# Kernel tuning notes

Measured on AMD Instinct MI355X. Metric: run time of the kernel, lower is better.

Reference implementation:

```python
import jax, jax.numpy as jnp
import numpy as np


def setup_inputs() -> dict:
    key = jax.random.key(0)
    ks = jax.random.split(key, 8)
    N, S, C, V = 64, 50, 100, 10000
    return {
        "logits": jax.random.normal(ks[0], (N, S, C), dtype=jnp.float32),
        "target": jax.random.randint(ks[1], (N, S), 0, V),
        "rel_candidate": jax.random.randint(ks[2], (N, S, C), 0, V),
        "rel_wordlist_num": V,
        "target_num": jax.random.randint(ks[3], (N,), 0, S),
        "rel_candidate_num": jax.random.randint(ks[4], (N, S), 0, C),
        "mask": jax.random.uniform(ks[5], (N, S), dtype=jnp.float32),
        "rel_weight": jax.random.uniform(ks[6], (N, S), dtype=jnp.float32),
    }


def reference(logits, target, rel_candidate, rel_wordlist_num, target_num,
              rel_candidate_num, mask, rel_weight):
    N, S, C = logits.shape
    V = rel_wordlist_num
    # validity of each (bs, rel_id, cand_id) triple per the nested-loop bounds
    valid = (jnp.arange(S)[None, :, None] < target_num[:, None, None]) & \
            (jnp.arange(C)[None, None, :] < rel_candidate_num[:, :, None])
    # route invalid entries to a dummy column V, then drop it
    idx = jnp.where(valid, rel_candidate, V)           # (N, S, C)
    b = jnp.arange(N)[:, None, None]
    s = jnp.arange(S)[None, :, None]
    logits_full = jnp.zeros((N, S, V + 1), logits.dtype).at[b, s, idx].set(logits)[..., :V]
    flat = logits_full.reshape(-1, V)                  # (N*S, V)
    tgt = target[:, :S].reshape(-1)
    # NLLLoss(reduce=False): loss_i = -input[i, target_i]
    loss = -jnp.take_along_axis(flat, tgt[:, None], axis=1)[:, 0]
    return jnp.sum(loss * rel_weight.reshape(-1)) / jnp.sum(mask.reshape(-1))
```

## Files before the change

kernel.cpp:

```cpp
#include <hip/hip_runtime.h>

#define NN 64
#define SS 50
#define CC 100
#define ROWS (NN * SS)
#define RPW 8
#define WPB 4
#define NBLK (ROWS / (RPW * WPB))

__global__ __launch_bounds__(256) void lmc_main(
    const float* __restrict__ logits,
    const int*   __restrict__ target,
    const int*   __restrict__ rel_candidate,
    const int*   __restrict__ target_num,
    const int*   __restrict__ rel_candidate_num,
    const float* __restrict__ mask,
    const float* __restrict__ rel_weight,
    double*      __restrict__ partial)
{
    const int tid  = threadIdx.x;
    const int lane = tid & 63;
    const int wid  = tid >> 6;
    const int row0 = blockIdx.x * (RPW * WPB) + wid * RPW;

    double num = 0.0;
    double den = (lane < RPW) ? (double)mask[row0 + lane] : 0.0;

    #pragma unroll
    for (int r = 0; r < RPW; ++r) {
        const int row = row0 + r;
        const int b   = row / SS;
        const int s   = row - b * SS;

        if (s < target_num[b]) {
            int cn = rel_candidate_num[row];
            if (cn > CC) cn = CC;
            const int tgt = target[row];
            const int* cand = rel_candidate + (size_t)row * CC;

            const int c0 = lane;
            const int c1 = lane + 64;
            const bool m0 = (c0 < cn) && (cand[c0] == tgt);
            const bool m1 = (c1 < CC) && (c1 < cn) && (cand[c1] == tgt);

            const unsigned long long bb1 = __ballot(m1);
            const unsigned long long bb0 = __ballot(m0);

            if (bb1) {
                const int win = 63 - __clzll(bb1);
                if (lane == win)
                    num += -(double)logits[(size_t)row * CC + c1] *
                            (double)rel_weight[row];
            } else if (bb0) {
                const int win = 63 - __clzll(bb0);
                if (lane == win)
                    num += -(double)logits[(size_t)row * CC + c0] *
                            (double)rel_weight[row];
            }
        }
    }

    __shared__ double s_num[256];
    __shared__ double s_den[256];
    s_num[tid] = num;
    s_den[tid] = den;
    __syncthreads();
    #pragma unroll
    for (int off = 128; off > 0; off >>= 1) {
        if (tid < off) {
            s_num[tid] += s_num[tid + off];
            s_den[tid] += s_den[tid + off];
        }
        __syncthreads();
    }
    if (tid == 0) {
        partial[2 * blockIdx.x]     = s_num[0];
        partial[2 * blockIdx.x + 1] = s_den[0];
    }
}

__global__ __launch_bounds__(128) void lmc_final(
    const double* __restrict__ partial, float* __restrict__ out)
{
    const int tid = threadIdx.x;
    double n = (tid < NBLK) ? partial[2 * tid]     : 0.0;
    double d = (tid < NBLK) ? partial[2 * tid + 1] : 0.0;
    __shared__ double sn[128];
    __shared__ double sd[128];
    sn[tid] = n;
    sd[tid] = d;
    __syncthreads();
    #pragma unroll
    for (int off = 64; off > 0; off >>= 1) {
        if (tid < off) {
            sn[tid] += sn[tid + off];
            sd[tid] += sd[tid + off];
        }
        __syncthreads();
    }
    if (tid == 0) out[0] = (float)(sn[0] / sd[0]);
}

extern "C" void kernel_launch(void* const* d_in, const int* in_sizes, int n_in,
                              void* d_out, int out_size, void* d_ws, size_t ws_size,
                              hipStream_t stream) {
    const float* logits            = (const float*)d_in[0];
    const int*   target            = (const int*)d_in[1];
    const int*   rel_candidate     = (const int*)d_in[2];
    const int*   target_num        = (const int*)d_in[4];
    const int*   rel_candidate_num = (const int*)d_in[5];
    const float* mask              = (const float*)d_in[6];
    const float* rel_weight        = (const float*)d_in[7];
    float*  out     = (float*)d_out;
    double* partial = (double*)d_ws;

    lmc_main<<<NBLK, 256, 0, stream>>>(logits, target, rel_candidate,
                                       target_num, rel_candidate_num,
                                       mask, rel_weight, partial);
    lmc_final<<<1, 128, 0, stream>>>(partial, out);
}
```

Baseline: 12.00 us.

## Fuse final reduction into main kernel via cooperative grid sync

Replaces the two-kernel launch with a single cooperative kernel: after writing per-block partials, all blocks do a grid-wide sync and block 0 reduces the partials and writes the output. Rows per wave are halved, which doubles the grid to 200 blocks so each block has less serial work. The aim is to drop the second kernel launch and its gap. In exchange it adds the cost of a grid barrier and a cooperative launch, which needs every block to be resident at once.

```diff
diff --git a/kernel.cpp b/kernel.cpp
--- a/kernel.cpp
+++ b/kernel.cpp
@@ -1,14 +1,17 @@
 #include <hip/hip_runtime.h>
+#include <hip/hip_cooperative_groups.h>
+
+namespace cg = cooperative_groups;
 
 #define NN 64
 #define SS 50
 #define CC 100
 #define ROWS (NN * SS)
-#define RPW 8
+#define RPW 4
 #define WPB 4
 #define NBLK (ROWS / (RPW * WPB))
 
-__global__ __launch_bounds__(256) void lmc_main(
+__global__ __launch_bounds__(256) void lmc_fused(
     const float* __restrict__ logits,
     const int*   __restrict__ target,
     const int*   __restrict__ rel_candidate,
@@ -16,7 +19,8 @@
     const int*   __restrict__ rel_candidate_num,
     const float* __restrict__ mask,
     const float* __restrict__ rel_weight,
-    double*      __restrict__ partial)
+    double*      __restrict__ partial,
+    float*       __restrict__ out)
 {
     const int tid  = threadIdx.x;
     const int lane = tid & 63;
@@ -77,28 +81,25 @@
         partial[2 * blockIdx.x]     = s_num[0];
         partial[2 * blockIdx.x + 1] = s_den[0];
     }
-}
 
-__global__ __launch_bounds__(128) void lmc_final(
-    const double* __restrict__ partial, float* __restrict__ out)
-{
-    const int tid = threadIdx.x;
-    double n = (tid < NBLK) ? partial[2 * tid]     : 0.0;
-    double d = (tid < NBLK) ? partial[2 * tid + 1] : 0.0;
-    __shared__ double sn[128];
-    __shared__ double sd[128];
-    sn[tid] = n;
-    sd[tid] = d;
-    __syncthreads();
-    #pragma unroll
-    for (int off = 64; off > 0; off >>= 1) {
-        if (tid < off) {
-            sn[tid] += sn[tid + off];
-            sd[tid] += sd[tid + off];
+    cg::this_grid().sync();
+
+    if (blockIdx.x == 0) {
+        double n = (tid < NBLK) ? partial[2 * tid]     : 0.0;
+        double d = (tid < NBLK) ? partial[2 * tid + 1] : 0.0;
+        s_num[tid] = n;
+        s_den[tid] = d;
+        __syncthreads();
+        #pragma unroll
+        for (int off = 128; off > 0; off >>= 1) {
+            if (tid < off) {
+                s_num[tid] += s_num[tid + off];
+                s_den[tid] += s_den[tid + off];
+            }
+            __syncthreads();
         }
-        __syncthreads();
+        if (tid == 0) out[0] = (float)(s_num[0] / s_den[0]);
     }
-    if (tid == 0) out[0] = (float)(sn[0] / sd[0]);
 }
 
 extern "C" void kernel_launch(void* const* d_in, const int* in_sizes, int n_in,
@@ -114,8 +115,11 @@
     float*  out     = (float*)d_out;
     double* partial = (double*)d_ws;
 
-    lmc_main<<<NBLK, 256, 0, stream>>>(logits, target, rel_candidate,
-                                       target_num, rel_candidate_num,
-                                       mask, rel_weight, partial);
-    lmc_final<<<1, 128, 0, stream>>>(partial, out);
+    void* args[] = {
+        (void*)&logits, (void*)&target, (void*)&rel_candidate,
+        (void*)&target_num, (void*)&rel_candidate_num,
+        (void*)&mask, (void*)&rel_weight, (void*)&partial, (void*)&out
+    };
+    hipLaunchCooperativeKernel((const void*)lmc_fused, dim3(NBLK), dim3(256),
+                               args, 0, stream);
 }
```

After: 46.18 us. +284.8%, slower.
